# Kernel optimization log

Measured on AMD Instinct MI355X. Metric: run time of the kernel, lower is better.

The kernel has to match this reference:

```python
import jax, jax.numpy as jnp
import numpy as np

EPS = 1e-7  # keras.backend.epsilon()
B, U, F = 1024, 256, 31
D = 1 + U + F  # features dim after concat


def setup_inputs() -> dict:
    key = jax.random.key(0)
    ks = jax.random.split(key, 9)
    s = 1.0 / np.sqrt(D)
    return {
        "last_cell": jax.random.uniform(ks[0], (B, U), dtype=jnp.float32),
        "input_precipitation": jax.random.uniform(ks[1], (B,), dtype=jnp.float32),
        "input_other_features": jax.random.normal(ks[2], (B, F), dtype=jnp.float32),
        "W_i": jax.random.normal(ks[3], (D, U), dtype=jnp.float32) * s,
        "b_i": jnp.zeros((U,), dtype=jnp.float32),
        "W_r": jax.random.normal(ks[4], (D, U * U), dtype=jnp.float32) * s,
        "b_r": jnp.zeros((U * U,), dtype=jnp.float32),
        "W_o": jax.random.normal(ks[5], (D, U), dtype=jnp.float32) * s,
        "b_o": jnp.zeros((U,), dtype=jnp.float32),
    }


def reference(last_cell, input_precipitation, input_other_features,
              W_i, b_i, W_r, b_r, W_o, b_o):
    # L1-normalize last cell state (mass fractions)
    l1 = jnp.sum(jnp.abs(last_cell), axis=-1, keepdims=True) + EPS
    last_cell_hat = last_cell / l1
    p = input_precipitation[:, None]  # [B,1]
    features = jnp.concatenate([p, last_cell_hat, input_other_features], axis=-1)  # [B,D]

    # input gate: sigmoid then L1-normalized across units (mass-conserving split)
    ig = jax.nn.sigmoid(features @ W_i + b_i)
    ig = ig / jnp.sum(jnp.abs(ig), axis=-1, keepdims=True)

    # redistribution matrix: relu, reshape [B,U,U], L1-normalize each row
    R = jax.nn.relu(features @ W_r + b_r).reshape(-1, U, U)
    R = R / jnp.sum(jnp.abs(R), axis=-1, keepdims=True)

    # output gate: sigmoid
    og = jax.nn.sigmoid(features @ W_o + b_o)

    cell_in = ig * p                                   # [B,U]
    cell_sys = jnp.einsum('bu,buv->bv', last_cell, R)  # batched (1xU)@(UxU)
    candidate = cell_in + cell_sys
    output = og * candidate
    cell = (1.0 - og) * candidate
    return (cell, output)
```

## Files before the change

### kernel.cpp

```cpp
#include <hip/hip_runtime.h>


#define EPS_L1 1e-7f

constexpr int BB  = 1024;
constexpr int U   = 256;
constexpr int F   = 31;
constexpr int D   = 1 + U + F;
constexpr int NBV = BB * U;
constexpr int NCH = D / 32;
constexpr int UIMGB = NCH * 16384;
constexpr size_t WTB_BYTES  = (size_t)258 * UIMGB;
constexpr size_t FEAT_BYTES = (size_t)BB * D * 2;
constexpr int PITCH = 260;

typedef float f32x4 __attribute__((ext_vector_type(4)));
typedef short bf16x8 __attribute__((ext_vector_type(8)));

__device__ __forceinline__ unsigned f2bf(float x) {
  union { float f; unsigned u; } v; v.f = x;
  unsigned r = v.u + 0x7FFFu + ((v.u >> 16) & 1u);
  return r >> 16;
}

#define GLDS16(gp, lp)                                                        \
  __builtin_amdgcn_global_load_lds(                                          \
      (const __attribute__((address_space(1))) void*)(gp),                   \
      (__attribute__((address_space(3))) void*)(lp), 16, 0, 0)

__global__ __launch_bounds__(256) void k_prep(
    const float* __restrict__ lc, const float* __restrict__ p,
    const float* __restrict__ other,
    const float* __restrict__ Wi, const float* __restrict__ Wr,
    const float* __restrict__ Wo,
    short* __restrict__ WtB, short* __restrict__ featImg,
    float* __restrict__ cell_sys) {
  __shared__ short lds[2][32 * PITCH];
  __shared__ float inv_s[64];
  const int bid = blockIdx.x, t = threadIdx.x;

  if (bid < 258) {
    const float* src; long ld;
    if (bid < 256)       { src = Wr + (size_t)bid * 256; ld = 65536; }
    else if (bid == 256) { src = Wi; ld = 256; }
    else                 { src = Wo; ld = 256; }
    short* dst = WtB + (size_t)bid * 73728;
    const int lane = t & 63, wave = t >> 6;
    const int g = lane >> 4, l15 = lane & 15;

    for (int c = 0; c < 9; ++c) {
      short* buf = lds[c & 1];
#pragma unroll
      for (int i = 0; i < 8; ++i) {
        const int f = i * 256 + t;
        const int row = f >> 6, col4 = f & 63;
        const float4 v = *(const float4*)(src + (size_t)(c * 32 + row) * ld + col4 * 4);
        const unsigned lo = f2bf(v.x) | (f2bf(v.y) << 16);
        const unsigned hi = f2bf(v.z) | (f2bf(v.w) << 16);
        unsigned* wp = (unsigned*)&buf[row * PITCH + col4 * 4];
        wp[0] = lo; wp[1] = hi;
      }
      __syncthreads();
#pragma unroll
      for (int i = 0; i < 4; ++i) {
        const int n0 = wave * 4 + i;
        bf16x8 h;
#pragma unroll
        for (int j = 0; j < 8; ++j)
          h[j] = buf[(g * 8 + j) * PITCH + n0 * 16 + l15];
        *(bf16x8*)(dst + (size_t)(c * 16 + n0) * 512 + lane * 8) = h;
      }
    }
  } else if (bid < 274) {
    const int mb = bid - 258;
    const int b0 = mb * 64;
    const int row = t >> 2, q = t & 3;
    const float4* lp = (const float4*)(lc + (size_t)(b0 + row) * 256 + q * 64);
    float s = 0.f;
#pragma unroll
    for (int j = 0; j < 16; ++j) {
      const float4 v = lp[j];
      s += fabsf(v.x) + fabsf(v.y) + fabsf(v.z) + fabsf(v.w);
    }
    s += __shfl_xor(s, 1, 64);
    s += __shfl_xor(s, 2, 64);
    if (q == 0) inv_s[row] = 1.f / (s + EPS_L1);
    __syncthreads();
#pragma unroll
    for (int i = 0; i < 9; ++i) {
      const int idx = i * 256 + t;
      const int reg = idx >> 6, l = idx & 63;
      const int c = reg >> 2, mt = reg & 3;
      const int lrow = mt * 16 + (l & 15);
      const int grow = b0 + lrow;
      const int k0 = c * 32 + (l >> 4) * 8;
      bf16x8 h;
#pragma unroll
      for (int j = 0; j < 8; ++j) {
        const int k = k0 + j;
        float v;
        if (k == 0) v = p[grow];
        else if (k <= 256) v = lc[(size_t)grow * 256 + (k - 1)] * inv_s[lrow];
        else v = other[(size_t)grow * 31 + (k - 257)];
        h[j] = (short)f2bf(v);
      }
      *(bf16x8*)(featImg + (size_t)mb * 18432 + (size_t)reg * 512 + l * 8) = h;
    }
  } else {
    float4* cs4 = (float4*)cell_sys;
    const int base = (bid - 274) * 8192 + t;
    const float4 z = {0.f, 0.f, 0.f, 0.f};
#pragma unroll
    for (int k2 = 0; k2 < 32; ++k2) cs4[base + k2 * 256] = z;
  }
}

__global__ __launch_bounds__(512, 2) void k_heavyR4(
    const short* __restrict__ featImg, const short* __restrict__ WtB,
    const float* __restrict__ lc, const float* __restrict__ br,
    float* __restrict__ cell_sys) {
  __shared__ short aT[36864];
  __shared__ float rsum[2][2][128];
  __shared__ float lcs[2][128];

  const int t = threadIdx.x, lane = t & 63, wave = t >> 6;
  const int rg = wave >> 1, cg = wave & 1;
  const int quad = lane >> 4, l15 = lane & 15;
  const int bid = blockIdx.x;
  const int Mb = bid >> 5, ug = bid & 31;
  const int b0 = Mb * 128, u0 = ug * 8;

  {
    const char* gA = (const char*)featImg + (size_t)Mb * 73728;
    char* lA = (char*)aT;
#pragma unroll
    for (int i = 0; i < 9; ++i)
      GLDS16(gA + i * 8192 + t * 16, lA + i * 8192 + t * 16);
  }

  const char* bptr = (const char*)WtB + (size_t)u0 * UIMGB + cg * 8192 + lane * 16;
  bf16x8 bc[8], bn[8];
#pragma unroll
  for (int n = 0; n < 8; ++n) bc[n] = *(const bf16x8*)(bptr + n * 1024);
  bptr += 16384;

  f32x4 acc[2][8], outa[2][8];
#pragma unroll
  for (int mt = 0; mt < 2; ++mt)
#pragma unroll
    for (int n = 0; n < 8; ++n)
#pragma unroll
      for (int r = 0; r < 4; ++r) { acc[mt][n][r] = 0.f; outa[mt][n][r] = 0.f; }

  const char* aB = (const char*)aT + (rg >> 1) * 36864 + (rg & 1) * 2048 + lane * 16;

  __syncthreads();

  bf16x8 a0 = *(const bf16x8*)(aB);
  bf16x8 a1 = *(const bf16x8*)(aB + 1024);

  float bv[8], lcv = 0.f;
  int c = 0, u = u0;

  for (int s = 0; s < 72; ++s) {
#pragma unroll
    for (int n = 0; n < 8; ++n) bn[n] = *(const bf16x8*)(bptr + n * 1024);
    bptr += 16384;
    if (c == 0) {
#pragma unroll
      for (int n = 0; n < 8; ++n)
        bv[n] = br[(size_t)u * 256 + cg * 128 + n * 16 + l15];
      if (t < 128) lcv = lc[(size_t)(b0 + t) * 256 + u];
    }
    const int cn = (c == 8) ? 0 : c + 1;
    const bf16x8 an0 = *(const bf16x8*)(aB + cn * 4096);
    const bf16x8 an1 = *(const bf16x8*)(aB + cn * 4096 + 1024);

#pragma unroll
    for (int n = 0; n < 8; ++n) {
      acc[0][n] = __builtin_amdgcn_mfma_f32_16x16x32_bf16(a0, bc[n], acc[0][n], 0, 0, 0);
      acc[1][n] = __builtin_amdgcn_mfma_f32_16x16x32_bf16(a1, bc[n], acc[1][n], 0, 0, 0);
    }
    a0 = an0; a1 = an1;
#pragma unroll
    for (int n = 0; n < 8; ++n) bc[n] = bn[n];

    if (c == 8) {
      const int ub = u & 1;
      float sm[2][4];
#pragma unroll
      for (int mt = 0; mt < 2; ++mt)
#pragma unroll
        for (int r = 0; r < 4; ++r) {
          float sv = 0.f;
#pragma unroll
          for (int n = 0; n < 8; ++n) {
            const float rv = fmaxf(acc[mt][n][r] + bv[n], 0.f);
            acc[mt][n][r] = rv;
            sv += rv;
          }
          sm[mt][r] = sv;
        }
#pragma unroll
      for (int m = 1; m < 16; m <<= 1)
#pragma unroll
        for (int mt = 0; mt < 2; ++mt)
#pragma unroll
          for (int r = 0; r < 4; ++r)
            sm[mt][r] += __shfl_xor(sm[mt][r], m, 64);
      if (l15 == 0) {
#pragma unroll
        for (int mt = 0; mt < 2; ++mt)
#pragma unroll
          for (int r = 0; r < 4; ++r)
            rsum[ub][cg][rg * 32 + mt * 16 + quad * 4 + r] = sm[mt][r];
      }
      if (t < 128) lcs[ub][t] = lcv;
      __syncthreads();
#pragma unroll
      for (int mt = 0; mt < 2; ++mt)
#pragma unroll
        for (int r = 0; r < 4; ++r) {
          const int row = rg * 32 + mt * 16 + quad * 4 + r;
          const float alpha = lcs[ub][row] / (rsum[ub][0][row] + rsum[ub][1][row]);
#pragma unroll
          for (int n = 0; n < 8; ++n) {
            outa[mt][n][r] = fmaf(alpha, acc[mt][n][r], outa[mt][n][r]);
            acc[mt][n][r] = 0.f;
          }
        }
      c = 0; ++u;
    } else {
      ++c;
    }
  }

#pragma unroll
  for (int mt = 0; mt < 2; ++mt)
#pragma unroll
    for (int r = 0; r < 4; ++r) {
      const int grow = b0 + rg * 32 + mt * 16 + quad * 4 + r;
#pragma unroll
      for (int n = 0; n < 8; ++n)
        atomicAdd(&cell_sys[(size_t)grow * 256 + cg * 128 + n * 16 + l15],
                  outa[mt][n][r]);
    }
}

__global__ __launch_bounds__(512, 2) void k_post(
    const short* __restrict__ featImg, const short* __restrict__ WtB,
    const float* __restrict__ bi, const float* __restrict__ bo,
    const float* __restrict__ p, const float* __restrict__ cell_sys,
    float* __restrict__ dout) {
  __shared__ short aT[18432];
  __shared__ float rsum[64][12];
  __shared__ float ps[64];

  const int t = threadIdx.x, lane = t & 63, cg = t >> 6;
  const int quad = lane >> 4, l15 = lane & 15;
  const int mb = blockIdx.x, b0 = mb * 64;

  {
    const char* gsrc = (const char*)featImg + (size_t)mb * 36864;
    char* lbase = (char*)aT;
#pragma unroll
    for (int i = 0; i < 5; ++i) {
      if (i * 8 + cg < 36) {
        const int off = i * 8192 + t * 16;
        GLDS16(gsrc + off, lbase + off);
      }
    }
  }
  if (t < 64) ps[t] = p[b0 + t];

  f32x4 acc[4][2];
#pragma unroll
  for (int mt = 0; mt < 4; ++mt)
#pragma unroll
    for (int n = 0; n < 2; ++n)
#pragma unroll
      for (int r = 0; r < 4; ++r) acc[mt][n][r] = 0.f;

  const char* bptr = (const char*)WtB + (size_t)256 * UIMGB + cg * 2048 + lane * 16;
  bf16x8 cb0 = *(const bf16x8*)(bptr);
  bf16x8 cb1 = *(const bf16x8*)(bptr + 1024);
  bf16x8 nb0 = *(const bf16x8*)(bptr + 16384);
  bf16x8 nb1 = *(const bf16x8*)(bptr + 16384 + 1024);
  bptr += 32768;

  __syncthreads();

  float ig0[4][4], ig1[4][4], og0[4][4], og1[4][4];

#pragma unroll
  for (int g = 0; g < 2; ++g) {
    const float* bias = (g == 0) ? bi : bo;
    const float bv0 = bias[cg * 32 + l15];
    const float bv1 = bias[cg * 32 + 16 + l15];
#pragma unroll
    for (int c = 0; c < 9; ++c) {
      const bf16x8 pb0 = *(const bf16x8*)(bptr);
      const bf16x8 pb1 = *(const bf16x8*)(bptr + 1024);
      bptr += 16384;
      const char* ab = (const char*)aT + c * 4096 + lane * 16;
      const bf16x8 a0 = *(const bf16x8*)(ab);
      const bf16x8 a1 = *(const bf16x8*)(ab + 1024);
      const bf16x8 a2 = *(const bf16x8*)(ab + 2048);
      const bf16x8 a3 = *(const bf16x8*)(ab + 3072);
      acc[0][0] = __builtin_amdgcn_mfma_f32_16x16x32_bf16(a0, cb0, acc[0][0], 0, 0, 0);
      acc[0][1] = __builtin_amdgcn_mfma_f32_16x16x32_bf16(a0, cb1, acc[0][1], 0, 0, 0);
      acc[1][0] = __builtin_amdgcn_mfma_f32_16x16x32_bf16(a1, cb0, acc[1][0], 0, 0, 0);
      acc[1][1] = __builtin_amdgcn_mfma_f32_16x16x32_bf16(a1, cb1, acc[1][1], 0, 0, 0);
      acc[2][0] = __builtin_amdgcn_mfma_f32_16x16x32_bf16(a2, cb0, acc[2][0], 0, 0, 0);
      acc[2][1] = __builtin_amdgcn_mfma_f32_16x16x32_bf16(a2, cb1, acc[2][1], 0, 0, 0);
      acc[3][0] = __builtin_amdgcn_mfma_f32_16x16x32_bf16(a3, cb0, acc[3][0], 0, 0, 0);
      acc[3][1] = __builtin_amdgcn_mfma_f32_16x16x32_bf16(a3, cb1, acc[3][1], 0, 0, 0);
      cb0 = nb0; cb1 = nb1; nb0 = pb0; nb1 = pb1;
    }

#pragma unroll
    for (int mt = 0; mt < 4; ++mt)
#pragma unroll
      for (int r = 0; r < 4; ++r) {
        const float v0 = 1.f / (1.f + __expf(-(acc[mt][0][r] + bv0)));
        const float v1 = 1.f / (1.f + __expf(-(acc[mt][1][r] + bv1)));
        if (g == 0) { ig0[mt][r] = v0; ig1[mt][r] = v1; }
        else        { og0[mt][r] = v0; og1[mt][r] = v1; }
        acc[mt][0][r] = 0.f;
        acc[mt][1][r] = 0.f;
      }

    if (g == 0) {
      float sm[4][4];
#pragma unroll
      for (int mt = 0; mt < 4; ++mt)
#pragma unroll
        for (int r = 0; r < 4; ++r) sm[mt][r] = ig0[mt][r] + ig1[mt][r];
#pragma unroll
      for (int m = 1; m < 16; m <<= 1)
#pragma unroll
        for (int mt = 0; mt < 4; ++mt)
#pragma unroll
          for (int r = 0; r < 4; ++r)
            sm[mt][r] += __shfl_xor(sm[mt][r], m, 64);
      if (l15 == 0) {
#pragma unroll
        for (int mt = 0; mt < 4; ++mt)
#pragma unroll
          for (int r = 0; r < 4; ++r)
            rsum[mt * 16 + quad * 4 + r][cg] = sm[mt][r];
      }
      __syncthreads();
#pragma unroll
      for (int mt = 0; mt < 4; ++mt)
#pragma unroll
        for (int r = 0; r < 4; ++r) {
          const int row = mt * 16 + quad * 4 + r;
          const float4 ra = *(const float4*)&rsum[row][0];
          const float4 rb = *(const float4*)&rsum[row][4];
          const float inv = 1.f / (((ra.x + ra.y) + (ra.z + ra.w)) +
                                   ((rb.x + rb.y) + (rb.z + rb.w)));
          ig0[mt][r] *= inv;
          ig1[mt][r] *= inv;
        }
    }
  }

#pragma unroll
  for (int mt = 0; mt < 4; ++mt)
#pragma unroll
    for (int r = 0; r < 4; ++r) {
      const int row = mt * 16 + quad * 4 + r;
      const float pr = ps[row];
      const size_t base = (size_t)(b0 + row) * 256 + cg * 32 + l15;
      {
        const float cand = fmaf(ig0[mt][r], pr, cell_sys[base]);
        dout[base] = (1.f - og0[mt][r]) * cand;
        dout[NBV + base] = og0[mt][r] * cand;
      }
      {
        const float cand = fmaf(ig1[mt][r], pr, cell_sys[base + 16]);
        dout[base + 16] = (1.f - og1[mt][r]) * cand;
        dout[NBV + base + 16] = og1[mt][r] * cand;
      }
    }
}

extern "C" void kernel_launch(void* const* d_in, const int* in_sizes, int n_in,
                              void* d_out, int out_size, void* d_ws, size_t ws_size,
                              hipStream_t stream) {
  const float* lc    = (const float*)d_in[0];
  const float* p     = (const float*)d_in[1];
  const float* other = (const float*)d_in[2];
  const float* Wi    = (const float*)d_in[3];
  const float* bi    = (const float*)d_in[4];
  const float* Wr    = (const float*)d_in[5];
  const float* br    = (const float*)d_in[6];
  const float* Wo    = (const float*)d_in[7];
  const float* bo    = (const float*)d_in[8];
  float* out = (float*)d_out;

  char* wsb = (char*)d_ws;
  short* WtB      = (short*)wsb;
  short* featImg  = (short*)(wsb + WTB_BYTES);
  float* cell_sys = (float*)(wsb + WTB_BYTES + FEAT_BYTES);

  k_prep<<<282, 256, 0, stream>>>(lc, p, other, Wi, Wr, Wo, WtB, featImg, cell_sys);
  k_heavyR4<<<256, 512, 0, stream>>>(featImg, WtB, lc, br, cell_sys);
  k_post<<<16, 512, 0, stream>>>(featImg, WtB, bi, bo, p, cell_sys, out);
}
```

Before: 221.7 us.

## Retile heavy R kernel to 4x4 MFMA tiles and split weight prep across more blocks

The heavy redistribution kernel now gives each wave a 64-row by 64-column tile (4x4 MFMA fragments) instead of 32x128. It keeps a three-deep register ring of B fragments and double-buffered A fragments, and uses a fully unrolled per-unit K loop. The intent is more operand reuse per fragment load and fewer global B loads per MFMA. The weight-conversion part of the prep kernel is spread over three times as many blocks, each handling three K chunks, to raise parallelism in that stage. The row-sum reduction now uses a 4-way LDS layout and a fast reciprocal, trading register pressure and a little precision for fewer loads.

```diff
diff --git a/kernel.cpp b/kernel.cpp
--- a/kernel.cpp
+++ b/kernel.cpp
@@ -28,6 +28,8 @@
       (const __attribute__((address_space(1))) void*)(gp),                   \
       (__attribute__((address_space(3))) void*)(lp), 16, 0, 0)
 
+#define MFMA16(a, b, c) __builtin_amdgcn_mfma_f32_16x16x32_bf16((a), (b), (c), 0, 0, 0)
+
 __global__ __launch_bounds__(256) void k_prep(
     const float* __restrict__ lc, const float* __restrict__ p,
     const float* __restrict__ other,
@@ -39,17 +41,20 @@
   __shared__ float inv_s[64];
   const int bid = blockIdx.x, t = threadIdx.x;
 
-  if (bid < 258) {
+  if (bid < 774) {
+    const int u = bid / 3, part = bid % 3;
     const float* src; long ld;
-    if (bid < 256)       { src = Wr + (size_t)bid * 256; ld = 65536; }
-    else if (bid == 256) { src = Wi; ld = 256; }
-    else                 { src = Wo; ld = 256; }
-    short* dst = WtB + (size_t)bid * 73728;
+    if (u < 256)       { src = Wr + (size_t)u * 256; ld = 65536; }
+    else if (u == 256) { src = Wi; ld = 256; }
+    else               { src = Wo; ld = 256; }
+    short* dst = WtB + (size_t)u * 73728;
     const int lane = t & 63, wave = t >> 6;
     const int g = lane >> 4, l15 = lane & 15;
 
-    for (int c = 0; c < 9; ++c) {
-      short* buf = lds[c & 1];
+#pragma unroll
+    for (int cc = 0; cc < 3; ++cc) {
+      const int c = part * 3 + cc;
+      short* buf = lds[cc & 1];
 #pragma unroll
       for (int i = 0; i < 8; ++i) {
         const int f = i * 256 + t;
@@ -70,9 +75,10 @@
           h[j] = buf[(g * 8 + j) * PITCH + n0 * 16 + l15];
         *(bf16x8*)(dst + (size_t)(c * 16 + n0) * 512 + lane * 8) = h;
       }
-    }
-  } else if (bid < 274) {
-    const int mb = bid - 258;
+      __syncthreads();
+    }
+  } else if (bid < 790) {
+    const int mb = bid - 774;
     const int b0 = mb * 64;
     const int row = t >> 2, q = t & 3;
     const float4* lp = (const float4*)(lc + (size_t)(b0 + row) * 256 + q * 64);
@@ -108,23 +114,23 @@
     }
   } else {
     float4* cs4 = (float4*)cell_sys;
-    const int base = (bid - 274) * 8192 + t;
+    const int base = (bid - 790) * 8192 + t;
     const float4 z = {0.f, 0.f, 0.f, 0.f};
 #pragma unroll
     for (int k2 = 0; k2 < 32; ++k2) cs4[base + k2 * 256] = z;
   }
 }
 
-__global__ __launch_bounds__(512, 2) void k_heavyR4(
+__global__ __launch_bounds__(512, 2) void k_heavyR5(
     const short* __restrict__ featImg, const short* __restrict__ WtB,
     const float* __restrict__ lc, const float* __restrict__ br,
     float* __restrict__ cell_sys) {
   __shared__ short aT[36864];
-  __shared__ float rsum[2][2][128];
+  __shared__ float rsum[2][128][4];
   __shared__ float lcs[2][128];
 
   const int t = threadIdx.x, lane = t & 63, wave = t >> 6;
-  const int rg = wave >> 1, cg = wave & 1;
+  const int cq = wave & 3, rh = wave >> 2;
   const int quad = lane >> 4, l15 = lane & 15;
   const int bid = blockIdx.x;
   const int Mb = bid >> 5, ug = bid & 31;
@@ -138,112 +144,115 @@
       GLDS16(gA + i * 8192 + t * 16, lA + i * 8192 + t * 16);
   }
 
-  const char* bptr = (const char*)WtB + (size_t)u0 * UIMGB + cg * 8192 + lane * 16;
-  bf16x8 bc[8], bn[8];
-#pragma unroll
-  for (int n = 0; n < 8; ++n) bc[n] = *(const bf16x8*)(bptr + n * 1024);
-  bptr += 16384;
-
-  f32x4 acc[2][8], outa[2][8];
-#pragma unroll
-  for (int mt = 0; mt < 2; ++mt)
-#pragma unroll
-    for (int n = 0; n < 8; ++n)
-#pragma unroll
-      for (int r = 0; r < 4; ++r) { acc[mt][n][r] = 0.f; outa[mt][n][r] = 0.f; }
-
-  const char* aB = (const char*)aT + (rg >> 1) * 36864 + (rg & 1) * 2048 + lane * 16;
+  const char* aB = (const char*)aT + rh * 36864 + lane * 16;
+  const char* bB = (const char*)WtB + (size_t)u0 * UIMGB + cq * 4096 + lane * 16;
+
+  f32x4 acc[4][4], outa[4][4];
+#pragma unroll
+  for (int m = 0; m < 4; ++m)
+#pragma unroll
+    for (int n = 0; n < 4; ++n)
+#pragma unroll
+      for (int r = 0; r < 4; ++r) { acc[m][n][r] = 0.f; outa[m][n][r] = 0.f; }
+
+  bf16x8 bfr[3][4];
+#pragma unroll
+  for (int n = 0; n < 4; ++n) bfr[0][n] = *(const bf16x8*)(bB + n * 1024);
+#pragma unroll
+  for (int n = 0; n < 4; ++n) bfr[1][n] = *(const bf16x8*)(bB + 16384 + n * 1024);
 
   __syncthreads();
 
-  bf16x8 a0 = *(const bf16x8*)(aB);
-  bf16x8 a1 = *(const bf16x8*)(aB + 1024);
-
-  float bv[8], lcv = 0.f;
-  int c = 0, u = u0;
-
-  for (int s = 0; s < 72; ++s) {
-#pragma unroll
-    for (int n = 0; n < 8; ++n) bn[n] = *(const bf16x8*)(bptr + n * 1024);
-    bptr += 16384;
-    if (c == 0) {
-#pragma unroll
-      for (int n = 0; n < 8; ++n)
-        bv[n] = br[(size_t)u * 256 + cg * 128 + n * 16 + l15];
-      if (t < 128) lcv = lc[(size_t)(b0 + t) * 256 + u];
-    }
-    const int cn = (c == 8) ? 0 : c + 1;
-    const bf16x8 an0 = *(const bf16x8*)(aB + cn * 4096);
-    const bf16x8 an1 = *(const bf16x8*)(aB + cn * 4096 + 1024);
-
-#pragma unroll
-    for (int n = 0; n < 8; ++n) {
-      acc[0][n] = __builtin_amdgcn_mfma_f32_16x16x32_bf16(a0, bc[n], acc[0][n], 0, 0, 0);
-      acc[1][n] = __builtin_amdgcn_mfma_f32_16x16x32_bf16(a1, bc[n], acc[1][n], 0, 0, 0);
-    }
-    a0 = an0; a1 = an1;
-#pragma unroll
-    for (int n = 0; n < 8; ++n) bc[n] = bn[n];
-
-    if (c == 8) {
-      const int ub = u & 1;
-      float sm[2][4];
-#pragma unroll
-      for (int mt = 0; mt < 2; ++mt)
-#pragma unroll
-        for (int r = 0; r < 4; ++r) {
-          float sv = 0.f;
-#pragma unroll
-          for (int n = 0; n < 8; ++n) {
-            const float rv = fmaxf(acc[mt][n][r] + bv[n], 0.f);
-            acc[mt][n][r] = rv;
-            sv += rv;
-          }
-          sm[mt][r] = sv;
+  bf16x8 afr[2][4];
+#pragma unroll
+  for (int m = 0; m < 4; ++m) afr[0][m] = *(const bf16x8*)(aB + m * 1024);
+
+  for (int uu = 0; uu < 8; ++uu) {
+    const int u = u0 + uu;
+    float bv[4];
+
+#pragma unroll
+    for (int c = 0; c < 9; ++c) {
+      if (c == 0) {
+#pragma unroll
+        for (int n = 0; n < 4; ++n)
+          bv[n] = br[(size_t)u * 256 + cq * 64 + n * 16 + l15];
+        if (t < 128) lcs[uu & 1][t] = lc[(size_t)(b0 + t) * 256 + u];
+      }
+#pragma unroll
+      for (int n = 0; n < 4; ++n)
+        bfr[(c + 2) % 3][n] = *(const bf16x8*)(bB + (c + 2) * 16384 + n * 1024);
+      if (c < 8) {
+#pragma unroll
+        for (int m = 0; m < 4; ++m)
+          afr[(c + 1) & 1][m] = *(const bf16x8*)(aB + (c + 1) * 4096 + m * 1024);
+      }
+#pragma unroll
+      for (int m = 0; m < 4; ++m)
+#pragma unroll
+        for (int n = 0; n < 4; ++n)
+          acc[m][n] = MFMA16(afr[c & 1][m], bfr[c % 3][n], acc[m][n]);
+    }
+    bB += UIMGB;
+
+#pragma unroll
+    for (int m = 0; m < 4; ++m) afr[0][m] = *(const bf16x8*)(aB + m * 1024);
+
+    const int ub = uu & 1;
+    float sm[4][4];
+#pragma unroll
+    for (int m = 0; m < 4; ++m)
+#pragma unroll
+      for (int r = 0; r < 4; ++r) {
+        float sv = 0.f;
+#pragma unroll
+        for (int n = 0; n < 4; ++n) {
+          const float rv = fmaxf(acc[m][n][r] + bv[n], 0.f);
+          acc[m][n][r] = rv;
+          sv += rv;
         }
-#pragma unroll
-      for (int m = 1; m < 16; m <<= 1)
-#pragma unroll
-        for (int mt = 0; mt < 2; ++mt)
-#pragma unroll
-          for (int r = 0; r < 4; ++r)
-            sm[mt][r] += __shfl_xor(sm[mt][r], m, 64);
-      if (l15 == 0) {
-#pragma unroll
-        for (int mt = 0; mt < 2; ++mt)
-#pragma unroll
-          for (int r = 0; r < 4; ++r)
-            rsum[ub][cg][rg * 32 + mt * 16 + quad * 4 + r] = sm[mt][r];
-      }
-      if (t < 128) lcs[ub][t] = lcv;
-      __syncthreads();
-#pragma unroll
-      for (int mt = 0; mt < 2; ++mt)
-#pragma unroll
-        for (int r = 0; r < 4; ++r) {
-          const int row = rg * 32 + mt * 16 + quad * 4 + r;
-          const float alpha = lcs[ub][row] / (rsum[ub][0][row] + rsum[ub][1][row]);
-#pragma unroll
-          for (int n = 0; n < 8; ++n) {
-            outa[mt][n][r] = fmaf(alpha, acc[mt][n][r], outa[mt][n][r]);
-            acc[mt][n][r] = 0.f;
-          }
+        sm[m][r] = sv;
+      }
+#pragma unroll
+    for (int msk = 1; msk < 16; msk <<= 1)
+#pragma unroll
+      for (int m = 0; m < 4; ++m)
+#pragma unroll
+        for (int r = 0; r < 4; ++r)
+          sm[m][r] += __shfl_xor(sm[m][r], msk, 64);
+    if (l15 == 0) {
+#pragma unroll
+      for (int m = 0; m < 4; ++m)
+#pragma unroll
+        for (int r = 0; r < 4; ++r)
+          rsum[ub][rh * 64 + m * 16 + quad * 4 + r][cq] = sm[m][r];
+    }
+    __syncthreads();
+#pragma unroll
+    for (int m = 0; m < 4; ++m)
+#pragma unroll
+      for (int r = 0; r < 4; ++r) {
+        const int row = rh * 64 + m * 16 + quad * 4 + r;
+        const float4 rv = *(const float4*)&rsum[ub][row][0];
+        const float tot = (rv.x + rv.y) + (rv.z + rv.w);
+        const float alpha = lcs[ub][row] * __builtin_amdgcn_rcpf(tot);
+#pragma unroll
+        for (int n = 0; n < 4; ++n) {
+          outa[m][n][r] = fmaf(alpha, acc[m][n][r], outa[m][n][r]);
+          acc[m][n][r] = 0.f;
         }
-      c = 0; ++u;
-    } else {
-      ++c;
-    }
+      }
   }
 
 #pragma unroll
-  for (int mt = 0; mt < 2; ++mt)
+  for (int m = 0; m < 4; ++m)
 #pragma unroll
     for (int r = 0; r < 4; ++r) {
-      const int grow = b0 + rg * 32 + mt * 16 + quad * 4 + r;
-#pragma unroll
-      for (int n = 0; n < 8; ++n)
-        atomicAdd(&cell_sys[(size_t)grow * 256 + cg * 128 + n * 16 + l15],
-                  outa[mt][n][r]);
+      const int grow = b0 + rh * 64 + m * 16 + quad * 4 + r;
+#pragma unroll
+      for (int n = 0; n < 4; ++n)
+        atomicAdd(&cell_sys[(size_t)grow * 256 + cq * 64 + n * 16 + l15],
+                  outa[m][n][r]);
     }
 }
 
@@ -307,14 +316,14 @@
       const bf16x8 a1 = *(const bf16x8*)(ab + 1024);
       const bf16x8 a2 = *(const bf16x8*)(ab + 2048);
       const bf16x8 a3 = *(const bf16x8*)(ab + 3072);
-      acc[0][0] = __builtin_amdgcn_mfma_f32_16x16x32_bf16(a0, cb0, acc[0][0], 0, 0, 0);
-      acc[0][1] = __builtin_amdgcn_mfma_f32_16x16x32_bf16(a0, cb1, acc[0][1], 0, 0, 0);
-      acc[1][0] = __builtin_amdgcn_mfma_f32_16x16x32_bf16(a1, cb0, acc[1][0], 0, 0, 0);
-      acc[1][1] = __builtin_amdgcn_mfma_f32_16x16x32_bf16(a1, cb1, acc[1][1], 0, 0, 0);
-      acc[2][0] = __builtin_amdgcn_mfma_f32_16x16x32_bf16(a2, cb0, acc[2][0], 0, 0, 0);
-      acc[2][1] = __builtin_amdgcn_mfma_f32_16x16x32_bf16(a2, cb1, acc[2][1], 0, 0, 0);
-      acc[3][0] = __builtin_amdgcn_mfma_f32_16x16x32_bf16(a3, cb0, acc[3][0], 0, 0, 0);
-      acc[3][1] = __builtin_amdgcn_mfma_f32_16x16x32_bf16(a3, cb1, acc[3][1], 0, 0, 0);
+      acc[0][0] = MFMA16(a0, cb0, acc[0][0]);
+      acc[0][1] = MFMA16(a0, cb1, acc[0][1]);
+      acc[1][0] = MFMA16(a1, cb0, acc[1][0]);
+      acc[1][1] = MFMA16(a1, cb1, acc[1][1]);
+      acc[2][0] = MFMA16(a2, cb0, acc[2][0]);
+      acc[2][1] = MFMA16(a2, cb1, acc[2][1]);
+      acc[3][0] = MFMA16(a3, cb0, acc[3][0]);
+      acc[3][1] = MFMA16(a3, cb1, acc[3][1]);
       cb0 = nb0; cb1 = nb1; nb0 = pb0; nb1 = pb1;
     }
 
@@ -337,12 +346,12 @@
 #pragma unroll
         for (int r = 0; r < 4; ++r) sm[mt][r] = ig0[mt][r] + ig1[mt][r];
 #pragma unroll
-      for (int m = 1; m < 16; m <<= 1)
+      for (int msk = 1; msk < 16; msk <<= 1)
 #pragma unroll
         for (int mt = 0; mt < 4; ++mt)
 #pragma unroll
           for (int r = 0; r < 4; ++r)
-            sm[mt][r] += __shfl_xor(sm[mt][r], m, 64);
+            sm[mt][r] += __shfl_xor(sm[mt][r], msk, 64);
       if (l15 == 0) {
 #pragma unroll
         for (int mt = 0; mt < 4; ++mt)
@@ -405,7 +414,7 @@
   short* featImg  = (short*)(wsb + WTB_BYTES);
   float* cell_sys = (float*)(wsb + WTB_BYTES + FEAT_BYTES);
 
-  k_prep<<<282, 256, 0, stream>>>(lc, p, other, Wi, Wr, Wo, WtB, featImg, cell_sys);
-  k_heavyR4<<<256, 512, 0, stream>>>(featImg, WtB, lc, br, cell_sys);
+  k_prep<<<798, 256, 0, stream>>>(lc, p, other, Wi, Wr, Wo, WtB, featImg, cell_sys);
+  k_heavyR5<<<256, 512, 0, stream>>>(featImg, WtB, lc, br, cell_sys);
   k_post<<<16, 512, 0, stream>>>(featImg, WtB, bi, bo, p, cell_sys, out);
 }
```

After: 220.6 us. Within noise of the previous version (-0.5%).
